# Performance work log

Hardware: AMD Instinct MI355X
Metric: run time of the kernel (lower is better)

The kernel has to match this reference:

```python
import jax, jax.numpy as jnp
import numpy as np

N_NODES = 50000
N_EDGES = 800000
F_IN, D1, N_CLS = 128, 128, 64


def gcn_conv(x, W, b, src, dst, n):
    # x: [N, Fin] -> linear transform then normalized scatter-add aggregation
    h = x @ W  # [N, Fout]
    deg = jnp.zeros((n,), h.dtype).at[dst].add(jnp.ones((dst.shape[0],), h.dtype))
    dis = jnp.where(deg > 0, jax.lax.rsqrt(jnp.maximum(deg, 1.0)), 0.0)  # deg^-1/2, inf->0
    norm = dis[src] * dis[dst]  # [E_tot]
    msgs = norm[:, None] * h[src]  # gather source features, scale by sym norm
    out = jax.ops.segment_sum(msgs, dst, num_segments=n)  # scatter-add to targets
    return out + b


def setup_inputs() -> dict:
    key = jax.random.key(0)
    ks = jax.random.split(key, 6)
    x = jax.random.normal(ks[0], (N_NODES, F_IN), dtype=jnp.float32)
    edge_index = jax.random.randint(ks[1], (2, N_EDGES), 0, N_NODES, dtype=jnp.int64)
    W1 = jax.random.normal(ks[2], (F_IN, D1), dtype=jnp.float32) / np.sqrt(F_IN)
    b1 = jnp.zeros((D1,), dtype=jnp.float32)
    W2 = jax.random.normal(ks[3], (D1, N_CLS), dtype=jnp.float32) / np.sqrt(D1)
    b2 = jnp.zeros((N_CLS,), dtype=jnp.float32)
    return {"x": x, "edge_index": edge_index, "W1": W1, "b1": b1, "W2": W2, "b2": b2}


def reference(x, edge_index, W1, b1, W2, b2):
    n = x.shape[0]
    loops = jnp.arange(n, dtype=edge_index.dtype)
    src = jnp.concatenate([edge_index[0], loops])  # add self-loops (PyG default)
    dst = jnp.concatenate([edge_index[1], loops])
    h = gcn_conv(x, W1, b1, src, dst, n)
    h = jax.nn.relu(h)
    # F.dropout(training=self.training) is identity in eval mode
    out = gcn_conv(h, W2, b2, src, dst, n)
    return out
```

## Files before the change

kernel.cpp:

```cpp
#include <hip/hip_runtime.h>

#define NN 50000
#define NE 800000
#define CAP 64
#define SLICE 6250

typedef unsigned int   u32;
typedef unsigned short u16;
typedef __attribute__((ext_vector_type(8))) short short8;
typedef __attribute__((ext_vector_type(4))) float f32x4;

__device__ inline u16 f2bf(float f) {
    u32 u = __float_as_uint(f);
    return (u16)((u + 0x7FFF + ((u >> 16) & 1)) >> 16);
}
__device__ inline float bfval(u16 h) { return __uint_as_float(((u32)h) << 16); }
__device__ inline float bf_lo(u32 u) { return __uint_as_float(u << 16); }
__device__ inline float bf_hi(u32 u) { return __uint_as_float(u & 0xFFFF0000u); }


__global__ __launch_bounds__(256) void build_ell(const int* __restrict__ ei,
                                                 int* __restrict__ cnt,
                                                 u16* __restrict__ ell) {
    const int s  = blockIdx.x & 7;
    const int g  = blockIdx.x >> 3;
    const int ng = gridDim.x >> 3;
    const int lo = s * SLICE, hi = lo + SLICE;
    for (int e0 = (g * 256 + (int)threadIdx.x) * 4; e0 < NE; e0 += ng * 1024) {
        int4 d4 = *(const int4*)(ei + NE + e0);
        int dv[4] = {d4.x, d4.y, d4.z, d4.w};
#pragma unroll
        for (int k = 0; k < 4; ++k) {
            int d = dv[k];
            if (d >= lo && d < hi) {
                int src = ei[e0 + k];
                int pos = atomicAdd(&cnt[d], 1);
                if (pos < CAP) ell[d * CAP + pos] = (u16)src;
            }
        }
    }
}


__global__ __launch_bounds__(256) void prep_w(const float* __restrict__ W1,
                                              const float* __restrict__ W2,
                                              u16* __restrict__ W1h, u16* __restrict__ W1l,
                                              u16* __restrict__ W2h, u16* __restrict__ W2l) {
    int i = blockIdx.x * 256 + threadIdx.x;
    const float* W; u16 *Dh, *Dl; int NOUT, idx;
    if (i < 16384) { W = W1; Dh = W1h; Dl = W1l; NOUT = 128; idx = i; }
    else           { idx = i - 16384; if (idx >= 8192) return;
                     W = W2; Dh = W2h; Dl = W2l; NOUT = 64; }
    int j = idx & 7, l = (idx >> 3) & 63, kc = (idx >> 9) & 3, t = idx >> 11;
    int k = kc * 32 + (l >> 4) * 8 + j;
    int n = t * 16 + (l & 15);
    float w = W[k * NOUT + n];
    u16 h = f2bf(w);
    Dh[idx] = h;
    Dl[idx] = f2bf(w - bfval(h));
}


template <int NOUT>
__global__ __launch_bounds__(256) void gemm_mfma(const float* __restrict__ A,
                                                 const u16* __restrict__ Wh,
                                                 const u16* __restrict__ Wl,
                                                 u16* __restrict__ C, int M) {
    constexpr int NT = NOUT / 16;
    const int tid = threadIdx.x;
    const int w = tid >> 6, l = tid & 63;
    const int m = l & 15, q = l >> 4;

    int arow = blockIdx.x * 64 + w * 16 + m;
    const float* Ar = A + (size_t)min(arow, M - 1) * 128;

    f32x4 acc[NT] = {};

#pragma unroll
    for (int kc = 0; kc < 4; ++kc) {
        float p[8];
        *(float4*)&p[0] = *(const float4*)(Ar + kc * 32 + q * 8);
        *(float4*)&p[4] = *(const float4*)(Ar + kc * 32 + q * 8 + 4);
        short8 ah, al;
#pragma unroll
        for (int j = 0; j < 8; ++j) {
            u16 h = f2bf(p[j]);
            ah[j] = (short)h;
            al[j] = (short)f2bf(p[j] - bfval(h));
        }
#pragma unroll
        for (int t = 0; t < NT; ++t) {
            size_t bo = ((size_t)(t * 4 + kc) * 64 + l) * 8;
            short8 bh = *(const short8*)(Wh + bo);
            short8 bl = *(const short8*)(Wl + bo);
            acc[t] = __builtin_amdgcn_mfma_f32_16x16x32_bf16(ah, bh, acc[t], 0, 0, 0);
            acc[t] = __builtin_amdgcn_mfma_f32_16x16x32_bf16(al, bh, acc[t], 0, 0, 0);
            acc[t] = __builtin_amdgcn_mfma_f32_16x16x32_bf16(ah, bl, acc[t], 0, 0, 0);
        }
    }

    int growbase = blockIdx.x * 64 + w * 16 + q * 4;
#pragma unroll
    for (int t = 0; t < NT; ++t)
#pragma unroll
        for (int r = 0; r < 4; ++r) {
            int grow = growbase + r;
            if (grow < M) C[(size_t)grow * NOUT + t * 16 + m] = f2bf(acc[t][r]);
        }
}


template <int F, bool RELU>
__global__ __launch_bounds__(256) void aggregate(const u16* __restrict__ H,
                                                 const u16* __restrict__ ell,
                                                 const int* __restrict__ cnt,
                                                 const float* __restrict__ bias,
                                                 float* __restrict__ out) {
    const int tid = threadIdx.x;
    const int node = (int)((blockIdx.x * 256 + tid) >> 6);
    if (node >= NN) return;
    const int lane = tid & 63;

    const int cn = cnt[node];
    const int ne = min(cn, 63);
    const float di = rsqrtf((float)(cn + 1));
    int   s_l = (lane < ne) ? (int)ell[(size_t)node * CAP + lane] : node;
    float n_l = (lane <= ne) ? rsqrtf((float)(cnt[s_l] + 1)) * di : 0.0f;

    constexpr int G = (F == 128) ? 4 : 8;
    constexpr int L = 64 / G;
    const int g = lane / L;
    const int ci = lane & (L - 1);

    const int m = ne + 1;
    const int mPad = (m + 2 * G - 1) & ~(2 * G - 1);

    float acc[8] = {0, 0, 0, 0, 0, 0, 0, 0};
    for (int j = 0; j < mPad; j += 2 * G) {
        int   sA = __shfl(s_l, j + g);
        float nA = __shfl(n_l, j + g);
        int   sB = __shfl(s_l, j + G + g);
        float nB = __shfl(n_l, j + G + g);
        uint4 vA = *(const uint4*)(H + (size_t)sA * F + ci * 8);
        uint4 vB = *(const uint4*)(H + (size_t)sB * F + ci * 8);
        acc[0] += nA * bf_lo(vA.x); acc[1] += nA * bf_hi(vA.x);
        acc[2] += nA * bf_lo(vA.y); acc[3] += nA * bf_hi(vA.y);
        acc[4] += nA * bf_lo(vA.z); acc[5] += nA * bf_hi(vA.z);
        acc[6] += nA * bf_lo(vA.w); acc[7] += nA * bf_hi(vA.w);
        acc[0] += nB * bf_lo(vB.x); acc[1] += nB * bf_hi(vB.x);
        acc[2] += nB * bf_lo(vB.y); acc[3] += nB * bf_hi(vB.y);
        acc[4] += nB * bf_lo(vB.z); acc[5] += nB * bf_hi(vB.z);
        acc[6] += nB * bf_lo(vB.w); acc[7] += nB * bf_hi(vB.w);
    }

#pragma unroll
    for (int i = 0; i < 8; ++i) {
        if (F == 64) acc[i] += __shfl_xor(acc[i], 8);
        acc[i] += __shfl_xor(acc[i], 16);
        acc[i] += __shfl_xor(acc[i], 32);
    }

    if (F == 128) {
        if (lane < 32) {
            int part = lane >> 4;
            int c0 = (lane & 15) * 8 + part * 4;
            float4 b4 = *(const float4*)(bias + c0);
            float4 o = make_float4(acc[part * 4 + 0] + b4.x, acc[part * 4 + 1] + b4.y,
                                   acc[part * 4 + 2] + b4.z, acc[part * 4 + 3] + b4.w);
            if (RELU) { o.x = fmaxf(o.x, 0.f); o.y = fmaxf(o.y, 0.f);
                        o.z = fmaxf(o.z, 0.f); o.w = fmaxf(o.w, 0.f); }
            *(float4*)(out + (size_t)node * 128 + c0) = o;
        }
    } else {
        if (lane < 16) {
            int part = (lane >> 3) & 1;
            int c0 = (lane & 7) * 8 + part * 4;
            float4 b4 = *(const float4*)(bias + c0);
            float4 o = make_float4(acc[part * 4 + 0] + b4.x, acc[part * 4 + 1] + b4.y,
                                   acc[part * 4 + 2] + b4.z, acc[part * 4 + 3] + b4.w);
            if (RELU) { o.x = fmaxf(o.x, 0.f); o.y = fmaxf(o.y, 0.f);
                        o.z = fmaxf(o.z, 0.f); o.w = fmaxf(o.w, 0.f); }
            *(float4*)(out + (size_t)node * 64 + c0) = o;
        }
    }
}


extern "C" void kernel_launch(void* const* d_in, const int* in_sizes, int n_in,
                              void* d_out, int out_size, void* d_ws, size_t ws_size,
                              hipStream_t stream) {
    const float* x  = (const float*)d_in[0];
    const int*   ei = (const int*)d_in[1];
    const float* W1 = (const float*)d_in[2];
    const float* b1 = (const float*)d_in[3];
    const float* W2 = (const float*)d_in[4];
    const float* b2 = (const float*)d_in[5];
    float* out = (float*)d_out;

    char* ws = (char*)d_ws;
    size_t off = 0;
    int* cnt = (int*)ws;                     off += (size_t)51200 * 4;
    u16* ell = (u16*)(ws + off);             off += (size_t)NN * CAP * 2;
    off = (off + 255) & ~(size_t)255;
    u16* W1h = (u16*)(ws + off);             off += 16384 * 2;
    u16* W1l = (u16*)(ws + off);             off += 16384 * 2;
    u16* W2h = (u16*)(ws + off);             off += 8192 * 2;
    u16* W2l = (u16*)(ws + off);             off += 8192 * 2;
    off = (off + 255) & ~(size_t)255;
    u16* Hbf = (u16*)(ws + off);             off += (size_t)NN * 128 * 2;
    float* bufB = (float*)(ws + off);        off += (size_t)NN * 128 * 4;

    hipMemsetAsync(cnt, 0, NN * sizeof(int), stream);
    prep_w<<<96, 256, 0, stream>>>(W1, W2, W1h, W1l, W2h, W2l);
    build_ell<<<1600, 256, 0, stream>>>(ei, cnt, ell);

    gemm_mfma<128><<<(NN + 63) / 64, 256, 0, stream>>>(x, W1h, W1l, Hbf, NN);
    aggregate<128, true><<<(NN + 3) / 4, 256, 0, stream>>>(Hbf, ell, cnt, b1, bufB);

    gemm_mfma<64><<<(NN + 63) / 64, 256, 0, stream>>>(bufB, W2h, W2l, Hbf, NN);
    aggregate<64, false><<<(NN + 3) / 4, 256, 0, stream>>>(Hbf, ell, cnt, b2, out);
}
```

Baseline: 202.7 us.

## Store hidden activations in bf16, split degree counters, fold memset into prep

The first aggregation now writes its ReLU output as bf16 instead of fp32. A new GEMM reads that bf16 input directly and drops the low-part A product, which halves the intermediate write and read traffic. Edge counters are split into two halves by edge parity to reduce atomic contention on each destination, and each node's ELL slots are split into two 32-entry sub-lists. The counter memset moves into prep_w, saving one launch. The trade-offs are extra bf16 rounding of the hidden layer, and overflow once either parity half exceeds 32 edges.

```diff
diff --git a/kernel.cpp b/kernel.cpp
--- a/kernel.cpp
+++ b/kernel.cpp
@@ -3,6 +3,7 @@
 #define NN 50000
 #define NE 800000
 #define CAP 64
+#define NPAD 50176
 #define SLICE 6250
 
 typedef unsigned int   u32;
@@ -34,8 +35,9 @@
             int d = dv[k];
             if (d >= lo && d < hi) {
                 int src = ei[e0 + k];
-                int pos = atomicAdd(&cnt[d], 1);
-                if (pos < CAP) ell[d * CAP + pos] = (u16)src;
+                int sh = k & 1;
+                int pos = atomicAdd(&cnt[sh * NPAD + d], 1);
+                if (pos < 32) ell[d * CAP + sh * 32 + pos] = (u16)src;
             }
         }
     }
@@ -45,8 +47,10 @@
 __global__ __launch_bounds__(256) void prep_w(const float* __restrict__ W1,
                                               const float* __restrict__ W2,
                                               u16* __restrict__ W1h, u16* __restrict__ W1l,
-                                              u16* __restrict__ W2h, u16* __restrict__ W2l) {
+                                              u16* __restrict__ W2h, u16* __restrict__ W2l,
+                                              int* __restrict__ cnt) {
     int i = blockIdx.x * 256 + threadIdx.x;
+    for (int z = i; z < 2 * NPAD; z += 32768) cnt[z] = 0;
     const float* W; u16 *Dh, *Dl; int NOUT, idx;
     if (i < 16384) { W = W1; Dh = W1h; Dl = W1l; NOUT = 128; idx = i; }
     else           { idx = i - 16384; if (idx >= 8192) return;
@@ -110,22 +114,64 @@
 }
 
 
-template <int F, bool RELU>
+__global__ __launch_bounds__(256) void gemm_mfma_bf(const u16* __restrict__ A,
+                                                    const u16* __restrict__ Wh,
+                                                    const u16* __restrict__ Wl,
+                                                    u16* __restrict__ C, int M) {
+    constexpr int NT = 4;
+    const int tid = threadIdx.x;
+    const int w = tid >> 6, l = tid & 63;
+    const int m = l & 15, q = l >> 4;
+
+    int arow = blockIdx.x * 64 + w * 16 + m;
+    const u16* Ar = A + (size_t)min(arow, M - 1) * 128;
+
+    f32x4 acc[NT] = {};
+
+#pragma unroll
+    for (int kc = 0; kc < 4; ++kc) {
+        short8 ah = *(const short8*)(Ar + kc * 32 + q * 8);
+#pragma unroll
+        for (int t = 0; t < NT; ++t) {
+            size_t bo = ((size_t)(t * 4 + kc) * 64 + l) * 8;
+            short8 bh = *(const short8*)(Wh + bo);
+            short8 bl = *(const short8*)(Wl + bo);
+            acc[t] = __builtin_amdgcn_mfma_f32_16x16x32_bf16(ah, bh, acc[t], 0, 0, 0);
+            acc[t] = __builtin_amdgcn_mfma_f32_16x16x32_bf16(ah, bl, acc[t], 0, 0, 0);
+        }
+    }
+
+    int growbase = blockIdx.x * 64 + w * 16 + q * 4;
+#pragma unroll
+    for (int t = 0; t < NT; ++t)
+#pragma unroll
+        for (int r = 0; r < 4; ++r) {
+            int grow = growbase + r;
+            if (grow < M) C[(size_t)grow * 64 + t * 16 + m] = f2bf(acc[t][r]);
+        }
+}
+
+
+template <int F, bool RELU, bool OUTBF>
 __global__ __launch_bounds__(256) void aggregate(const u16* __restrict__ H,
                                                  const u16* __restrict__ ell,
                                                  const int* __restrict__ cnt,
                                                  const float* __restrict__ bias,
-                                                 float* __restrict__ out) {
+                                                 void* __restrict__ outp) {
     const int tid = threadIdx.x;
     const int node = (int)((blockIdx.x * 256 + tid) >> 6);
     if (node >= NN) return;
     const int lane = tid & 63;
 
-    const int cn = cnt[node];
-    const int ne = min(cn, 63);
-    const float di = rsqrtf((float)(cn + 1));
-    int   s_l = (lane < ne) ? (int)ell[(size_t)node * CAP + lane] : node;
-    float n_l = (lane <= ne) ? rsqrtf((float)(cnt[s_l] + 1)) * di : 0.0f;
+    const int c0r = cnt[node], c1r = cnt[NPAD + node];
+    const int c0 = min(c0r, 32), c1 = min(c1r, 32);
+    const int ne = min(c0 + c1, 63);
+    const float di = rsqrtf((float)(c0r + c1r + 1));
+    int slot = (lane < c0) ? lane : 32 + (lane - c0);
+    int   s_l = (lane < ne) ? (int)ell[(size_t)node * CAP + slot] : node;
+    float n_l = (lane <= ne)
+                    ? rsqrtf((float)(cnt[s_l] + cnt[NPAD + s_l] + 1)) * di
+                    : 0.0f;
 
     constexpr int G = (F == 128) ? 4 : 8;
     constexpr int L = 64 / G;
@@ -160,27 +206,23 @@
         acc[i] += __shfl_xor(acc[i], 32);
     }
 
-    if (F == 128) {
-        if (lane < 32) {
-            int part = lane >> 4;
-            int c0 = (lane & 15) * 8 + part * 4;
-            float4 b4 = *(const float4*)(bias + c0);
-            float4 o = make_float4(acc[part * 4 + 0] + b4.x, acc[part * 4 + 1] + b4.y,
-                                   acc[part * 4 + 2] + b4.z, acc[part * 4 + 3] + b4.w);
-            if (RELU) { o.x = fmaxf(o.x, 0.f); o.y = fmaxf(o.y, 0.f);
-                        o.z = fmaxf(o.z, 0.f); o.w = fmaxf(o.w, 0.f); }
-            *(float4*)(out + (size_t)node * 128 + c0) = o;
-        }
-    } else {
-        if (lane < 16) {
-            int part = (lane >> 3) & 1;
-            int c0 = (lane & 7) * 8 + part * 4;
-            float4 b4 = *(const float4*)(bias + c0);
-            float4 o = make_float4(acc[part * 4 + 0] + b4.x, acc[part * 4 + 1] + b4.y,
-                                   acc[part * 4 + 2] + b4.z, acc[part * 4 + 3] + b4.w);
-            if (RELU) { o.x = fmaxf(o.x, 0.f); o.y = fmaxf(o.y, 0.f);
-                        o.z = fmaxf(o.z, 0.f); o.w = fmaxf(o.w, 0.f); }
-            *(float4*)(out + (size_t)node * 64 + c0) = o;
+    const int active = (F == 128) ? 32 : 16;
+    if (lane < active) {
+        int part, c0i;
+        if (F == 128) { part = lane >> 4;       c0i = (lane & 15) * 8 + part * 4; }
+        else          { part = (lane >> 3) & 1; c0i = (lane & 7) * 8 + part * 4; }
+        float4 b4 = *(const float4*)(bias + c0i);
+        float4 o = make_float4(acc[part * 4 + 0] + b4.x, acc[part * 4 + 1] + b4.y,
+                               acc[part * 4 + 2] + b4.z, acc[part * 4 + 3] + b4.w);
+        if (RELU) { o.x = fmaxf(o.x, 0.f); o.y = fmaxf(o.y, 0.f);
+                    o.z = fmaxf(o.z, 0.f); o.w = fmaxf(o.w, 0.f); }
+        if (OUTBF) {
+            u16* out = (u16*)outp;
+            *(ushort4*)(out + (size_t)node * F + c0i) =
+                make_ushort4(f2bf(o.x), f2bf(o.y), f2bf(o.z), f2bf(o.w));
+        } else {
+            float* out = (float*)outp;
+            *(float4*)(out + (size_t)node * F + c0i) = o;
         }
     }
 }
@@ -199,7 +241,7 @@
 
     char* ws = (char*)d_ws;
     size_t off = 0;
-    int* cnt = (int*)ws;                     off += (size_t)51200 * 4;
+    int* cnt = (int*)ws;                     off += (size_t)2 * NPAD * 4;
     u16* ell = (u16*)(ws + off);             off += (size_t)NN * CAP * 2;
     off = (off + 255) & ~(size_t)255;
     u16* W1h = (u16*)(ws + off);             off += 16384 * 2;
@@ -208,15 +250,14 @@
     u16* W2l = (u16*)(ws + off);             off += 8192 * 2;
     off = (off + 255) & ~(size_t)255;
     u16* Hbf = (u16*)(ws + off);             off += (size_t)NN * 128 * 2;
-    float* bufB = (float*)(ws + off);        off += (size_t)NN * 128 * 4;
-
-    hipMemsetAsync(cnt, 0, NN * sizeof(int), stream);
-    prep_w<<<96, 256, 0, stream>>>(W1, W2, W1h, W1l, W2h, W2l);
+    u16* Abf = (u16*)(ws + off);             off += (size_t)NN * 128 * 2;
+
+    prep_w<<<128, 256, 0, stream>>>(W1, W2, W1h, W1l, W2h, W2l, cnt);
     build_ell<<<1600, 256, 0, stream>>>(ei, cnt, ell);
 
     gemm_mfma<128><<<(NN + 63) / 64, 256, 0, stream>>>(x, W1h, W1l, Hbf, NN);
-    aggregate<128, true><<<(NN + 3) / 4, 256, 0, stream>>>(Hbf, ell, cnt, b1, bufB);
-
-    gemm_mfma<64><<<(NN + 63) / 64, 256, 0, stream>>>(bufB, W2h, W2l, Hbf, NN);
-    aggregate<64, false><<<(NN + 3) / 4, 256, 0, stream>>>(Hbf, ell, cnt, b2, out);
-}
+    aggregate<128, true, true><<<(NN + 3) / 4, 256, 0, stream>>>(Hbf, ell, cnt, b1, Abf);
+
+    gemm_mfma_bf<<<(NN + 63) / 64, 256, 0, stream>>>(Abf, W2h, W2l, Hbf, NN);
+    aggregate<64, false, false><<<(NN + 3) / 4, 256, 0, stream>>>(Hbf, ell, cnt, b2, out);
+}
```

Measured after the change: 196.9 us. -2.8%, faster.
